# Optimization experiments

Measured on AMD Instinct MI355X. Metric: run time of the kernel, lower is better.

The kernel has to match this reference:

```python
import jax, jax.numpy as jnp
import numpy as np

B, H, W = 256, 512, 512
KH, KW = 16, 16
OH, OW = 8, 8
N = (H // KH) * (W // KW)  # 1024 chunks
KIN = KH * KW              # 256
KOUT = OH * OW             # 64


def setup_inputs() -> dict:
    key = jax.random.key(0)
    kx, kw, kb = jax.random.split(key, 3)
    x = jax.random.normal(kx, (B, H, W), dtype=jnp.float32)
    # Per-chunk Linear weights, torch-style uniform(-1/sqrt(fan_in), 1/sqrt(fan_in))
    bound = 1.0 / np.sqrt(KIN)
    Wk = jax.random.uniform(kw, (N, KOUT, KIN), dtype=jnp.float32, minval=-bound, maxval=bound)
    bk = jax.random.uniform(kb, (N, KOUT), dtype=jnp.float32, minval=-bound, maxval=bound)
    return {"x": x, "Wk": Wk, "bk": bk}


def _split_chunks(x):
    # [B,H,W] -> [B, N, KH, KW] matching split_matrix_in_chunks
    b = x.shape[0]
    return (x.reshape(b, H // KH, KH, W // KW, KW)
             .swapaxes(2, 3)
             .reshape(b, N, KH, KW))


def _recombine(chunks):
    # [B, N, OH, OW] -> [B, s*OH, s*OW] matching recombine_chunks_into_matrix
    b = chunks.shape[0]
    s = int(np.sqrt(N))
    return (chunks.reshape(b, s, s, OH, OW)
                  .swapaxes(3, 2)
                  .reshape(b, s * OH, s * OW))


def reference(x, Wk, bk):
    xc = _split_chunks(x).reshape(-1, N, KIN)          # [B,N,KIN]
    # grouped GEMM: one Linear per chunk, fused with bias + ReLU
    y = jnp.einsum('bnk,nok->bno', xc, Wk) + bk[None]  # [B,N,KOUT]
    y = jax.nn.relu(y)
    out = _recombine(y.reshape(-1, N, OH, OW))         # [B, s*OH, s*OW]
    b, h, w = out.shape
    return out.reshape(b, h * w)
```

## Files before the change

kernel.cpp:

```cpp
#include <hip/hip_runtime.h>


typedef __bf16 bf16x8 __attribute__((ext_vector_type(8)));
typedef float  f32x4  __attribute__((ext_vector_type(4)));

constexpr int LDW = 264;

union bfpack {
  unsigned short s[8];
  bf16x8 v;
};

__device__ __forceinline__ unsigned short f2bf(float f) {
  union { float f; unsigned u; } v; v.f = f;
  unsigned r = v.u + 0x7fffu + ((v.u >> 16) & 1u);
  return (unsigned short)(r >> 16);
}

__global__ __launch_bounds__(256, 4) void comp_kernel(
    const float* __restrict__ x, const float* __restrict__ Wk,
    const float* __restrict__ bk, float* __restrict__ out) {
  __shared__ unsigned short Ws[64 * LDW];
  __shared__ float bs[64];

  const int bid = blockIdx.x;
  const int n  = ((bid & 7) << 7) | (bid >> 3);
  const int ci = n >> 5, cj = n & 31;
  const int t = threadIdx.x;
  const int wave = t >> 6, lane = t & 63;
  const int m15 = lane & 15, quad = lane >> 4;

  const float4* wsrc = (const float4*)(Wk + (size_t)n * (64 * 256));
  #pragma unroll
  for (int it = 0; it < 8; ++it) {
    int i2 = it * 512 + t * 2;
    float4 g0 = wsrc[i2];
    float4 g1 = wsrc[i2 + 1];
    int o = i2 >> 6, pos = (i2 & 63) * 4;
    bfpack p;
    p.s[0] = f2bf(g0.x); p.s[1] = f2bf(g0.y); p.s[2] = f2bf(g0.z); p.s[3] = f2bf(g0.w);
    p.s[4] = f2bf(g1.x); p.s[5] = f2bf(g1.y); p.s[6] = f2bf(g1.z); p.s[7] = f2bf(g1.w);
    *(bf16x8*)&Ws[o * LDW + pos] = p.v;
  }
  if (t < 64) bs[t] = bk[n * 64 + t];
  __syncthreads();

  const float* xb = x + (size_t)(ci * 16) * 512 + cj * 16
                      + (quad >> 1) * 512 + (quad & 1) * 8;

  for (int bp = 0; bp < 4; ++bp) {
    const int btile = bp * 64 + wave * 16;
    const float* xp = xb + (size_t)(btile + m15) * (512 * 512);
    f32x4 acc[4] = {{0,0,0,0},{0,0,0,0},{0,0,0,0},{0,0,0,0}};

    #pragma unroll
    for (int ks = 0; ks < 8; ++ks) {
      float4 v0 = *(const float4*)(xp + ks * 1024);
      float4 v1 = *(const float4*)(xp + ks * 1024 + 4);
      bfpack a;
      a.s[0] = f2bf(v0.x); a.s[1] = f2bf(v0.y); a.s[2] = f2bf(v0.z); a.s[3] = f2bf(v0.w);
      a.s[4] = f2bf(v1.x); a.s[5] = f2bf(v1.y); a.s[6] = f2bf(v1.z); a.s[7] = f2bf(v1.w);

      const int ka = ks * 32 + quad * 8;
      bf16x8 bb[4];
      #pragma unroll
      for (int nt = 0; nt < 4; ++nt)
        bb[nt] = *(const bf16x8*)&Ws[(nt * 16 + m15) * LDW + ka];
      #pragma unroll
      for (int nt = 0; nt < 4; ++nt)
        acc[nt] = __builtin_amdgcn_mfma_f32_16x16x32_bf16(a.v, bb[nt], acc[nt], 0, 0, 0);
    }

    #pragma unroll
    for (int nt = 0; nt < 4; ++nt) {
      int o = nt * 16 + m15;
      float bias = bs[o];
      size_t obase = (size_t)(ci * 8 + (o >> 3)) * 256 + (size_t)(cj * 8 + (o & 7));
      #pragma unroll
      for (int r = 0; r < 4; ++r) {
        float val = acc[nt][r] + bias;
        val = val > 0.f ? val : 0.f;
        size_t bg = (size_t)(btile + quad * 4 + r);
        out[bg * 65536 + obase] = val;
      }
    }
  }
}

extern "C" void kernel_launch(void* const* d_in, const int* in_sizes, int n_in,
                              void* d_out, int out_size, void* d_ws, size_t ws_size,
                              hipStream_t stream) {
  const float* x  = (const float*)d_in[0];
  const float* Wk = (const float*)d_in[1];
  const float* bk = (const float*)d_in[2];
  float* out = (float*)d_out;
  comp_kernel<<<dim3(1024), dim3(256), 0, stream>>>(x, Wk, bk, out);
}
```

Before: 481.4 us.

## Pre-convert weights to bf16 fragments and stream x rows into LDS asynchronously

Adds a prepass kernel that converts the per-chunk weights to bf16 once, stored in MFMA fragment order in the workspace. The main kernel now assigns each block a chunk row and a slice of 16 batch rows. It double-buffers swizzled x rows into LDS with global_load_lds and prefetches the weight fragments into registers, overlapping loads with the MFMAs. Output is written as float4 with the bias added from LDS. This targets the scattered uncoalesced x reads and the repeated per-block weight conversion, at the cost of an extra kernel launch, a bf16 weight copy in the workspace, and heavy register use from the prefetched fragments.

```diff
diff --git a/kernel.cpp b/kernel.cpp
--- a/kernel.cpp
+++ b/kernel.cpp
@@ -4,12 +4,7 @@
 typedef __bf16 bf16x8 __attribute__((ext_vector_type(8)));
 typedef float  f32x4  __attribute__((ext_vector_type(4)));
 
-constexpr int LDW = 264;
-
-union bfpack {
-  unsigned short s[8];
-  bf16x8 v;
-};
+union bfpack { unsigned short s[8]; bf16x8 v; };
 
 __device__ __forceinline__ unsigned short f2bf(float f) {
   union { float f; unsigned u; } v; v.f = f;
@@ -17,72 +12,136 @@
   return (unsigned short)(r >> 16);
 }
 
-__global__ __launch_bounds__(256, 4) void comp_kernel(
-    const float* __restrict__ x, const float* __restrict__ Wk,
+typedef __attribute__((address_space(1))) const void GV;
+typedef __attribute__((address_space(3))) void LV;
+
+__global__ __launch_bounds__(256) void wconv_kernel(
+    const float* __restrict__ Wk, unsigned short* __restrict__ Wc) {
+  __shared__ unsigned short F[64 * 264];
+  const int n = blockIdx.x, t = threadIdx.x;
+  const float4* src = (const float4*)(Wk + (size_t)n * 16384);
+  #pragma unroll
+  for (int it = 0; it < 16; ++it) {
+    const int idx = it * 256 + t;
+    float4 g = src[idx];
+    const int o = idx >> 6, k0 = (idx & 63) * 4;
+    ushort4 p; p.x = f2bf(g.x); p.y = f2bf(g.y); p.z = f2bf(g.z); p.w = f2bf(g.w);
+    *(ushort4*)&F[o * 264 + k0] = p;
+  }
+  __syncthreads();
+  unsigned short* dst = Wc + (size_t)n * 16384;
+  #pragma unroll
+  for (int it = 0; it < 8; ++it) {
+    const int g = it * 256 + t;
+    const int ks = g >> 8, nt = (g >> 6) & 3, q = (g >> 4) & 3, o15 = g & 15;
+    *(uint4*)&dst[(size_t)g * 8] =
+        *(const uint4*)&F[(nt * 16 + o15) * 264 + ks * 32 + q * 8];
+  }
+}
+
+__global__ __launch_bounds__(512, 2) void comp_kernel(
+    const float* __restrict__ x, const unsigned short* __restrict__ Wc,
     const float* __restrict__ bk, float* __restrict__ out) {
-  __shared__ unsigned short Ws[64 * LDW];
-  __shared__ float bs[64];
+  __shared__ __align__(16) char Xs[2][16][4096];
+  __shared__ float bs[2048];
 
   const int bid = blockIdx.x;
-  const int n  = ((bid & 7) << 7) | (bid >> 3);
-  const int ci = n >> 5, cj = n & 31;
-  const int t = threadIdx.x;
-  const int wave = t >> 6, lane = t & 63;
+  const int xcd = bid & 7, j = bid >> 3;
+  const int ci  = xcd * 4 + (j >> 4);
+  const int bsl = j & 15;
+  const int t = threadIdx.x, wave = t >> 6, lane = t & 63;
   const int m15 = lane & 15, quad = lane >> 4;
 
-  const float4* wsrc = (const float4*)(Wk + (size_t)n * (64 * 256));
+  float4 bfrag = *(const float4*)(bk + (size_t)ci * 2048 + t * 4);
+  *(float4*)&bs[t * 4] = bfrag;
+
+  const char* xrow = (const char*)x + (size_t)ci * 32768;
+
+  auto stage_issue = [&](int khp) {
+    char* db = &Xs[khp & 1][0][0];
+    #pragma unroll
+    for (int i = 0; i < 8; ++i) {
+      const int bl = 2 * wave + (i >> 2);
+      const int off = (i & 3) * 1024 + lane * 16;
+      const char* src = xrow + (size_t)(bsl * 16 + bl) * 1048576 + khp * 4096
+                        + (off ^ ((bl & 7) << 4));
+      __builtin_amdgcn_global_load_lds((GV*)src, (LV*)(db + bl * 4096 + off),
+                                       16, 0, 0);
+    }
+  };
+
+  const unsigned short* wp = Wc + (size_t)(ci * 32 + wave * 4) * 16384 + lane * 8;
+  bf16x8 bwA[4][4], bwB[4][4];
+  auto wload = [&](int khp, bf16x8 (*bw)[4]) {
+    #pragma unroll
+    for (int c = 0; c < 4; ++c)
+      #pragma unroll
+      for (int nt = 0; nt < 4; ++nt)
+        bw[c][nt] = *(const bf16x8*)(wp + (size_t)c * 16384 + khp * 2048 + nt * 512);
+  };
+
+  stage_issue(0); wload(0, bwA);
+  stage_issue(1); wload(1, bwB);
+  __builtin_amdgcn_sched_barrier(0);
+
+  f32x4 acc[4][4];
   #pragma unroll
-  for (int it = 0; it < 8; ++it) {
-    int i2 = it * 512 + t * 2;
-    float4 g0 = wsrc[i2];
-    float4 g1 = wsrc[i2 + 1];
-    int o = i2 >> 6, pos = (i2 & 63) * 4;
-    bfpack p;
-    p.s[0] = f2bf(g0.x); p.s[1] = f2bf(g0.y); p.s[2] = f2bf(g0.z); p.s[3] = f2bf(g0.w);
-    p.s[4] = f2bf(g1.x); p.s[5] = f2bf(g1.y); p.s[6] = f2bf(g1.z); p.s[7] = f2bf(g1.w);
-    *(bf16x8*)&Ws[o * LDW + pos] = p.v;
-  }
-  if (t < 64) bs[t] = bk[n * 64 + t];
-  __syncthreads();
+  for (int c = 0; c < 4; ++c)
+    #pragma unroll
+    for (int nt = 0; nt < 4; ++nt) acc[c][nt] = (f32x4){0, 0, 0, 0};
 
-  const float* xb = x + (size_t)(ci * 16) * 512 + cj * 16
-                      + (quad >> 1) * 512 + (quad & 1) * 8;
+  const int key = (m15 & 7) << 4;
 
-  for (int bp = 0; bp < 4; ++bp) {
-    const int btile = bp * 64 + wave * 16;
-    const float* xp = xb + (size_t)(btile + m15) * (512 * 512);
-    f32x4 acc[4] = {{0,0,0,0},{0,0,0,0},{0,0,0,0},{0,0,0,0}};
+  #pragma unroll
+  for (int khp = 0; khp < 8; ++khp) {
+    if (khp < 7) asm volatile("s_waitcnt vmcnt(40)" ::: "memory");
+    else         asm volatile("s_waitcnt vmcnt(16)" ::: "memory");
+    __builtin_amdgcn_sched_barrier(0);
+    __builtin_amdgcn_s_barrier();
 
+    bf16x8 (*bw)[4] = (khp & 1) ? bwB : bwA;
+    const char* Xb = &Xs[khp & 1][m15][0];
     #pragma unroll
-    for (int ks = 0; ks < 8; ++ks) {
-      float4 v0 = *(const float4*)(xp + ks * 1024);
-      float4 v1 = *(const float4*)(xp + ks * 1024 + 4);
+    for (int c = 0; c < 4; ++c) {
+      const int cj = wave * 4 + c;
+      const int r0 = (quad >> 1) * 2048 + cj * 64 + (quad & 1) * 32;
+      float4 v0 = *(const float4*)(Xb + ((r0)      ^ key));
+      float4 v1 = *(const float4*)(Xb + ((r0 + 16) ^ key));
       bfpack a;
       a.s[0] = f2bf(v0.x); a.s[1] = f2bf(v0.y); a.s[2] = f2bf(v0.z); a.s[3] = f2bf(v0.w);
       a.s[4] = f2bf(v1.x); a.s[5] = f2bf(v1.y); a.s[6] = f2bf(v1.z); a.s[7] = f2bf(v1.w);
-
-      const int ka = ks * 32 + quad * 8;
-      bf16x8 bb[4];
       #pragma unroll
       for (int nt = 0; nt < 4; ++nt)
-        bb[nt] = *(const bf16x8*)&Ws[(nt * 16 + m15) * LDW + ka];
-      #pragma unroll
-      for (int nt = 0; nt < 4; ++nt)
-        acc[nt] = __builtin_amdgcn_mfma_f32_16x16x32_bf16(a.v, bb[nt], acc[nt], 0, 0, 0);
+        acc[c][nt] = __builtin_amdgcn_mfma_f32_16x16x32_bf16(bw[c][nt], a.v, acc[c][nt], 0, 0, 0);
     }
 
+    asm volatile("s_waitcnt lgkmcnt(0)" ::: "memory");
+    __builtin_amdgcn_sched_barrier(0);
+    __builtin_amdgcn_s_barrier();
+
+    if (khp < 6) {
+      __builtin_amdgcn_sched_barrier(0);
+      stage_issue(khp + 2);
+      wload(khp + 2, (khp & 1) ? bwB : bwA);
+      __builtin_amdgcn_sched_barrier(0);
+    }
+  }
+
+  const int bg = bsl * 16 + m15;
+  float* op = out + (size_t)bg * 65536 + (size_t)(ci * 8) * 256;
+  #pragma unroll
+  for (int c = 0; c < 4; ++c) {
+    const int cj = wave * 4 + c;
     #pragma unroll
     for (int nt = 0; nt < 4; ++nt) {
-      int o = nt * 16 + m15;
-      float bias = bs[o];
-      size_t obase = (size_t)(ci * 8 + (o >> 3)) * 256 + (size_t)(cj * 8 + (o & 7));
-      #pragma unroll
-      for (int r = 0; r < 4; ++r) {
-        float val = acc[nt][r] + bias;
-        val = val > 0.f ? val : 0.f;
-        size_t bg = (size_t)(btile + quad * 4 + r);
-        out[bg * 65536 + obase] = val;
-      }
+      const int o0 = nt * 16 + quad * 4;
+      float4 b4 = *(const float4*)&bs[cj * 64 + o0];
+      float4 res;
+      res.x = fmaxf(acc[c][nt][0] + b4.x, 0.f);
+      res.y = fmaxf(acc[c][nt][1] + b4.y, 0.f);
+      res.z = fmaxf(acc[c][nt][2] + b4.z, 0.f);
+      res.w = fmaxf(acc[c][nt][3] + b4.w, 0.f);
+      *(float4*)&op[(o0 >> 3) * 256 + cj * 8 + (o0 & 7)] = res;
     }
   }
 }
@@ -94,5 +153,7 @@
   const float* Wk = (const float*)d_in[1];
   const float* bk = (const float*)d_in[2];
   float* out = (float*)d_out;
-  comp_kernel<<<dim3(1024), dim3(256), 0, stream>>>(x, Wk, bk, out);
+  unsigned short* Wc = (unsigned short*)d_ws;
+  wconv_kernel<<<dim3(1024), dim3(256), 0, stream>>>(Wk, Wc);
+  comp_kernel<<<dim3(512), dim3(512), 0, stream>>>(x, Wc, bk, out);
 }
```

Measured after the change: 444.2 us. 7.7% less time.
